# Optimization experiments

Measured on AMD Instinct MI355X. Metric: run time of the kernel, lower is better.

## Reference

```python
import jax, jax.numpy as jnp
import numpy as np

N = 5
C = 256
B, H, W = 8, 64, 64


def setup_inputs() -> dict:
    key = jax.random.key(0)
    ks = jax.random.split(key, 9)
    s = 0.05
    return {
        "inputs": jax.random.normal(ks[0], (B, N, C, H, W), dtype=jnp.float32),
        # grouped 1x1 conv: groups = N-1, each group maps C channels -> 1 channel, no bias
        "wgt_w": jax.random.normal(ks[1], (N - 1, C), dtype=jnp.float32) * s,
        # ConvGRU 1x1 gate convs: in = 2*C (cat of input and hidden), out = C, with bias
        "w_r": jax.random.normal(ks[2], (C, 2 * C), dtype=jnp.float32) * s,
        "b_r": jnp.zeros((C,), dtype=jnp.float32),
        "w_u": jax.random.normal(ks[3], (C, 2 * C), dtype=jnp.float32) * s,
        "b_u": jnp.zeros((C,), dtype=jnp.float32),
        "w_o": jax.random.normal(ks[4], (C, 2 * C), dtype=jnp.float32) * s,
        "b_o": jnp.zeros((C,), dtype=jnp.float32),
        "gamma": jax.random.normal(ks[5], (1,), dtype=jnp.float32) * s,
    }


def _conv1x1(x, Wm, bias):
    # x: [b, cin, h, w]; Wm: [cout, cin]
    return jnp.einsum("bchw,oc->bohw", x, Wm) + bias[None, :, None, None]


def reference(inputs, wgt_w, w_r, b_r, w_u, b_u, w_o, b_o, gamma):
    b, n, c, h, w = inputs.shape

    def gru(x, hprev):
        s = jnp.concatenate([x, hprev], axis=1)  # [b, 2c, h, w]
        u = jax.nn.sigmoid(_conv1x1(s, w_u, b_u))
        r = jax.nn.sigmoid(_conv1x1(s, w_r, b_r))
        o = jnp.tanh(_conv1x1(jnp.concatenate([x, hprev * r], axis=1), w_o, b_o))
        return hprev * (1.0 - u) + o * u

    preds = []
    for i in range(n):
        h_t = inputs[:, i]  # [b, c, h, w]
        idx = [j for j in range(n) if j != i]
        h_n = inputs[:, jnp.array(idx)]  # [b, n-1, c, h, w], neighbor-major channel layout
        diff = h_t[:, None] - h_n  # repeat(h_t, n-1) - cat(neighbors)
        # grouped 1x1 conv (groups = n-1, no bias): per-neighbor channel reduction
        wgt = jnp.einsum("bjchw,jc->bjhw", diff, wgt_w)  # [b, n-1, h, w]
        gate = jax.nn.sigmoid(wgt)
        # torch: wgt.unsqueeze(1).repeat(1, c, 1, 1, 1).view(b, c*(n-1), h, w)
        # -> flat channel index = cc*(n-1) + j  (note: differs from x2's j*c + cc layout)
        gate_full = jnp.broadcast_to(gate[:, None], (b, c, n - 1, h, w)).reshape(
            b, c * (n - 1), h, w
        )
        x2 = h_n.reshape(b, (n - 1) * c, h, w)
        msg = x2 * gate_full
        m_t = msg.reshape(b, n - 1, c, h, w).sum(axis=1)  # sum-aggregate over neighbors
        h_new = gru(m_t, h_t)
        preds.append(h_new * gamma + h_t)
    return jnp.stack(preds, axis=1)  # [b, n, c, h, w]
```

## Files before the change

kernel.cpp:

```cpp
#include <hip/hip_runtime.h>

typedef __attribute__((ext_vector_type(8))) short short8;
typedef __attribute__((ext_vector_type(4))) float f32x4;
typedef __attribute__((ext_vector_type(8))) unsigned short us8;
typedef __attribute__((ext_vector_type(4))) unsigned short us4;
typedef __attribute__((ext_vector_type(2))) unsigned short us2;

__device__ __forceinline__ float sigmoidf_(float x){ return 1.f/(1.f+__expf(-x)); }
__device__ __forceinline__ unsigned short f2bf(float f){
    union{float f; unsigned int u;} x; x.f = f;
    unsigned int r = x.u + 0x7fffu + ((x.u>>16)&1u);
    return (unsigned short)(r>>16);
}
__device__ __forceinline__ float bf2f(unsigned short u){
    union{unsigned int u; float f;} x; x.u = ((unsigned int)u)<<16; return x.f;
}
#define GAS(p) ((const __attribute__((address_space(1))) void*)(uintptr_t)(p))
#define LAS(p) ((__attribute__((address_space(3))) void*)(uintptr_t)(p))

#define SLOT 8388608ull

__global__ __launch_bounds__(256) void k_dots(const float* __restrict__ inp, const float* __restrict__ wgt,
                                              float* __restrict__ D){
    __shared__ float wg[1024];
    for (int s=threadIdx.x; s<1024; s+=256) wg[s] = wgt[s];
    __syncthreads();
    int e = blockIdx.x*256 + threadIdx.x;
    int pl = e & 4095;
    int bn = e >> 12;
    const float* base = inp + (((size_t)bn*256)<<12) + pl;
    float d0=0,d1=0,d2=0,d3=0;
    #pragma unroll 8
    for (int c=0;c<256;c++){
        float v = base[(size_t)c<<12];
        d0 += v*wg[c]; d1 += v*wg[256+c]; d2 += v*wg[512+c]; d3 += v*wg[768+c];
    }
    size_t o = ((size_t)bn*4)<<12;
    D[o+pl]=d0; D[o+4096+pl]=d1; D[o+8192+pl]=d2; D[o+12288+pl]=d3;
}

__global__ __launch_bounds__(256) void k_wp2(const float* __restrict__ w_u, const float* __restrict__ w_r,
                                             const float* __restrict__ w_o,
                                             unsigned short* __restrict__ Wc0, unsigned short* __restrict__ Wc1){
    int bx = blockIdx.x;
    const float *s0, *s1; unsigned short* dst; int OCN, tid;
    if (bx < 256){ tid = bx*256 + threadIdx.x; OCN = 512; s0 = w_u; s1 = w_r; dst = Wc0; }
    else         { tid = (bx-256)*256 + threadIdx.x; OCN = 256; s0 = w_o; s1 = w_o; dst = Wc1; }
    int d = tid*4;
    int kk = d & 63;
    int row = d >> 6;
    int oc = row & (OCN-1);
    int kb = row / OCN;
    int k  = kb*64 + kk;
    const float* src = (oc < 256) ? s0 : s1;
    int ocr = (oc < 256) ? oc : oc-256;
    float4 v = *(const float4*)&src[(size_t)ocr*512 + k];
    us4 pk; pk.x=f2bf(v.x); pk.y=f2bf(v.y); pk.z=f2bf(v.z); pk.w=f2bf(v.w);
    *(us4*)&dst[d] = pk;
}

__global__ __launch_bounds__(256) void k_bxs(const float* __restrict__ inp, const float* __restrict__ D,
                                             unsigned short* __restrict__ Alo, unsigned short* __restrict__ Ahi,
                                             int i0, int cnt){
    __shared__ unsigned short tm[64*34];
    __shared__ unsigned short th[64*34];
    int t  = threadIdx.x;
    int c0 = (blockIdx.x & 3) << 6;
    int pz = blockIdx.x >> 2;
    int p0 = pz << 5;
    int b  = p0 >> 12, pl0 = p0 & 4095;

    f32x4 x[5][2], S4[2];
    #pragma unroll
    for (int q=0;q<2;q++){
        int s = t + q*256;
        int c = s >> 3, pc = (s&7) << 2;
        int cc = c0 + c;
        f32x4 acc = {0.f,0.f,0.f,0.f};
        #pragma unroll
        for (int n=0;n<5;n++){
            x[n][q] = *(const f32x4*)&inp[(((size_t)((b*5+n)*256+cc))<<12) + pl0 + pc];
            acc += x[n][q];
        }
        S4[q] = acc;
    }
    int kb = c0 >> 6;
    #pragma unroll
    for (int i=0;i<5;i++){
        if (i < i0 || i >= i0+cnt) continue;
        #pragma unroll
        for (int q=0;q<2;q++){
            int s = t + q*256;
            int c = s >> 3, pc = (s&7) << 2;
            int j = c & 3;
            int node = (j < i) ? j : (j+1);
            f32x4 dw = *(const f32x4*)&D[(((size_t)((b*5+i)*4+j))<<12) + pl0 + pc];
            f32x4 dn = *(const f32x4*)&D[(((size_t)((b*5+node)*4+j))<<12) + pl0 + pc];
            f32x4 xi = x[i][q];
            f32x4 md = S4[q] - xi;
            int lb = c*34 + pc;
            us2 m0, m1, h0, h1;
            m0.x = f2bf(sigmoidf_(dw.x-dn.x)*md.x); m0.y = f2bf(sigmoidf_(dw.y-dn.y)*md.y);
            m1.x = f2bf(sigmoidf_(dw.z-dn.z)*md.z); m1.y = f2bf(sigmoidf_(dw.w-dn.w)*md.w);
            h0.x = f2bf(xi.x); h0.y = f2bf(xi.y); h1.x = f2bf(xi.z); h1.y = f2bf(xi.w);
            *(us2*)&tm[lb] = m0; *(us2*)&tm[lb+2] = m1;
            *(us2*)&th[lb] = h0; *(us2*)&th[lb+2] = h1;
        }
        __syncthreads();
        {
            int p = t >> 3, cs = (t&7) << 3;
            us8 vm, vh;
            #pragma unroll
            for (int j8=0;j8<8;j8++){ vm[j8] = tm[(cs+j8)*34 + p]; vh[j8] = th[(cs+j8)*34 + p]; }
            size_t dst = (size_t)(i - i0)*SLOT + ((size_t)kb*32768 + p0 + p)*64 + cs;
            *(us8*)&Alo[dst] = vm;
            *(us8*)&Ahi[dst] = vh;
        }
        __syncthreads();
    }
}

template<int EPI>
__global__ __launch_bounds__(256) void k_mm(
        const unsigned short* __restrict__ Alo, const unsigned short* __restrict__ Ahi,
        const unsigned short* __restrict__ Wb,
        const float* __restrict__ inp, const float* __restrict__ b0, const float* __restrict__ b1,
        unsigned short* __restrict__ U, unsigned short* __restrict__ A1hi, float* __restrict__ outp,
        const float* __restrict__ gamma_p, int i0)
{
    constexpr int OCN = EPI ? 256 : 512;
    __shared__ unsigned short As[128*64];
    __shared__ unsigned short Bs[128*64];
    int t  = threadIdx.x, wv = t>>6, ln = t&63;
    int p0 = blockIdx.x*128, oc0 = blockIdx.y*128;
    int z  = blockIdx.z, i = i0 + z;
    size_t zo = (size_t)z*SLOT;
    int wm = (wv>>1)*64, wn = (wv&1)*64;
    int row = ln & 15, quad = ln >> 4, kq = quad*8;

    f32x4 acc[4][4];
    f32x4 zr = {0.f,0.f,0.f,0.f};
    #pragma unroll
    for (int a=0;a<4;a++){
        #pragma unroll
        for (int o=0;o<4;o++) acc[a][o]=zr;
    }

    for (int kb=0; kb<8; ++kb){
        const unsigned short* gA = (kb<4) ? (Alo + zo + ((size_t)kb*32768 + p0)*64)
                                          : (Ahi + zo + ((size_t)(kb-4)*32768 + p0)*64);
        const unsigned short* gW = Wb + ((size_t)kb*OCN + oc0)*64;
        #pragma unroll
        for (int q=0;q<4;q++){
            int off = (wv*4+q)*512;
            __builtin_amdgcn_global_load_lds(GAS(gA + off + ln*8), LAS(Bs + off + ln*8), 16, 0, 0);
            __builtin_amdgcn_global_load_lds(GAS(gW + off + ln*8), LAS(As + off + ln*8), 16, 0, 0);
        }
        __syncthreads();
        #pragma unroll
        for (int ks=0; ks<2; ks++){
            short8 a[4], b[4];
            #pragma unroll
            for (int f=0; f<4; f++){
                a[f] = *(const short8*)&As[(wm+f*16+row)*64 + ks*32 + kq];
                b[f] = *(const short8*)&Bs[(wn+f*16+row)*64 + ks*32 + kq];
            }
            #pragma unroll
            for (int fm=0; fm<4; fm++){
                #pragma unroll
                for (int fn=0; fn<4; fn++)
                    acc[fm][fn] = __builtin_amdgcn_mfma_f32_16x16x32_bf16(a[fm], b[fn], acc[fm][fn], 0,0,0);
            }
        }
        __syncthreads();
    }

    float gm = EPI ? gamma_p[0] : 0.f;
    #pragma unroll
    for (int fn=0; fn<4; fn++){
        int p  = p0 + wn + fn*16 + row;
        int b  = p >> 12, pl = p & 4095;
        size_t hb = (((size_t)((b*5+i)*256))<<12) + pl;
        #pragma unroll
        for (int fm=0; fm<4; fm++){
            int ocb = oc0 + wm + fm*16 + quad*4;
            if (EPI==0){
                if (oc0 < 256){
                    #pragma unroll
                    for (int r=0;r<4;r++){
                        int oc = ocb + r;
                        U[zo + (size_t)oc*32768 + p] = f2bf(sigmoidf_(acc[fm][fn][r] + b0[oc]));
                    }
                } else {
                    int kb2 = ocb - 256;
                    size_t aidx = zo + ((size_t)(kb2>>6)*32768 + p)*64 + (kb2&63);
                    us4 vh = *(const us4*)&Ahi[aidx];
                    us4 pk;
                    #pragma unroll
                    for (int r=0;r<4;r++){
                        float rg = sigmoidf_(acc[fm][fn][r] + b1[kb2+r]);
                        pk[r] = f2bf(rg * bf2f(vh[r]));
                    }
                    *(us4*)&A1hi[aidx] = pk;
                }
            } else {
                #pragma unroll
                for (int r=0;r<4;r++){
                    int oc = ocb + r;
                    float v  = acc[fm][fn][r] + b0[oc];
                    float e2 = __expf(2.f*v);
                    float thv = 1.f - 2.f/(e2+1.f);
                    float u  = bf2f(U[zo + (size_t)oc*32768 + p]);
                    float h  = inp[hb + ((size_t)oc<<12)];
                    float hn = h*(1.f-u) + thv*u;
                    outp[hb + ((size_t)oc<<12)] = hn*gm + h;
                }
            }
        }
    }
}

extern "C" void kernel_launch(void* const* d_in, const int* in_sizes, int n_in,
                              void* d_out, int out_size, void* d_ws, size_t ws_size,
                              hipStream_t stream) {
    const float* inputs = (const float*)d_in[0];
    const float* wgt_w  = (const float*)d_in[1];
    const float* w_r    = (const float*)d_in[2];
    const float* b_r    = (const float*)d_in[3];
    const float* w_u    = (const float*)d_in[4];
    const float* b_u    = (const float*)d_in[5];
    const float* w_o    = (const float*)d_in[6];
    const float* b_o    = (const float*)d_in[7];
    const float* gamma  = (const float*)d_in[8];
    float* out = (float*)d_out;

    float* D = (float*)d_ws;
    unsigned short* Wc0 = (unsigned short*)(D + 655360);
    unsigned short* Wc1 = Wc0 + 262144;
    unsigned short* U   = Wc1 + 131072;

    size_t fixedB = 655360ull*4 + (262144ull + 131072ull)*2;
    size_t slotB  = 4ull*SLOT*2;
    int nb = 1;
    for (int k2=5;k2>=1;k2--){ if (fixedB + (size_t)k2*slotB <= ws_size){ nb = k2; break; } }

    unsigned short* Alo  = U   + (size_t)nb*SLOT;
    unsigned short* Ahi  = Alo + (size_t)nb*SLOT;
    unsigned short* A1hi = Ahi + (size_t)nb*SLOT;

    k_dots<<<640, 256, 0, stream>>>(inputs, wgt_w, D);
    k_wp2 <<<384, 256, 0, stream>>>(w_u, w_r, w_o, Wc0, Wc1);
    for (int i0=0; i0<5; i0+=nb){
        int cnt = (5-i0 < nb) ? (5-i0) : nb;
        k_bxs<<<4096, 256, 0, stream>>>(inputs, D, Alo, Ahi, i0, cnt);
        k_mm<0><<<dim3(256,4,cnt), 256, 0, stream>>>(Alo, Ahi, Wc0, inputs, b_u, b_r,
                                                     U, A1hi, nullptr, gamma, i0);
        k_mm<1><<<dim3(256,2,cnt), 256, 0, stream>>>(Alo, A1hi, Wc1, inputs, b_o, nullptr,
                                                     U, nullptr, out, gamma, i0);
    }
}
```

Before: 872.9 us.

## Double-buffer GEMM LDS tiles, XOR-swizzle layouts, remap blocks across XCDs, vectorize U

The GEMM kernel now double-buffers its LDS tiles so the next K-block loads while MFMAs run, and raises wave priority around the MFMA bursts. The weight and activation panels are XOR-swizzled when written, with matching swizzled LDS reads, to cut bank conflicts. A 1D grid is remapped so consecutive work tiles land on the same XCD, for better L2 sharing of operands. The U gate buffer is transposed to pixel-major so it can be stored and loaded as packed 4-wide vectors. Together these double LDS use and add index arithmetic, and any mismatch between writer and reader swizzles would produce wrong results.

```diff
diff --git a/kernel.cpp b/kernel.cpp
--- a/kernel.cpp
+++ b/kernel.cpp
@@ -56,7 +56,8 @@
     int ocr = (oc < 256) ? oc : oc-256;
     float4 v = *(const float4*)&src[(size_t)ocr*512 + k];
     us4 pk; pk.x=f2bf(v.x); pk.y=f2bf(v.y); pk.z=f2bf(v.z); pk.w=f2bf(v.w);
-    *(us4*)&dst[d] = pk;
+    int kk_sw = kk ^ ((oc&7)<<3);
+    *(us4*)&dst[(size_t)row*64 + kk_sw] = pk;
 }
 
 __global__ __launch_bounds__(256) void k_bxs(const float* __restrict__ inp, const float* __restrict__ D,
@@ -112,7 +113,8 @@
             us8 vm, vh;
             #pragma unroll
             for (int j8=0;j8<8;j8++){ vm[j8] = tm[(cs+j8)*34 + p]; vh[j8] = th[(cs+j8)*34 + p]; }
-            size_t dst = (size_t)(i - i0)*SLOT + ((size_t)kb*32768 + p0 + p)*64 + cs;
+            int cs_sw = cs ^ ((p&7)<<3);
+            size_t dst = (size_t)(i - i0)*SLOT + ((size_t)kb*32768 + p0 + p)*64 + cs_sw;
             *(us8*)&Alo[dst] = vm;
             *(us8*)&Ahi[dst] = vh;
         }
@@ -129,10 +131,17 @@
         const float* __restrict__ gamma_p, int i0)
 {
     constexpr int OCN = EPI ? 256 : 512;
-    __shared__ unsigned short As[128*64];
-    __shared__ unsigned short Bs[128*64];
+    constexpr int NY  = EPI ? 2   : 4;
+    constexpr int NWG = 256*NY;
+    __shared__ unsigned short As[2][128*64];
+    __shared__ unsigned short Bs[2][128*64];
     int t  = threadIdx.x, wv = t>>6, ln = t&63;
-    int p0 = blockIdx.x*128, oc0 = blockIdx.y*128;
+
+    int bid = blockIdx.x;
+    int wg  = (bid&7)*(NWG>>3) + (bid>>3);
+    int oc0 = (wg & (NY-1)) * 128;
+    int p0  = (wg / NY) * 128;
+
     int z  = blockIdx.z, i = i0 + z;
     size_t zo = (size_t)z*SLOT;
     int wm = (wv>>1)*64, wn = (wv&1)*64;
@@ -146,31 +155,42 @@
         for (int o=0;o<4;o++) acc[a][o]=zr;
     }
 
-    for (int kb=0; kb<8; ++kb){
+    auto stage = [&](int kb, int buf){
         const unsigned short* gA = (kb<4) ? (Alo + zo + ((size_t)kb*32768 + p0)*64)
                                           : (Ahi + zo + ((size_t)(kb-4)*32768 + p0)*64);
         const unsigned short* gW = Wb + ((size_t)kb*OCN + oc0)*64;
         #pragma unroll
         for (int q=0;q<4;q++){
             int off = (wv*4+q)*512;
-            __builtin_amdgcn_global_load_lds(GAS(gA + off + ln*8), LAS(Bs + off + ln*8), 16, 0, 0);
-            __builtin_amdgcn_global_load_lds(GAS(gW + off + ln*8), LAS(As + off + ln*8), 16, 0, 0);
-        }
-        __syncthreads();
+            __builtin_amdgcn_global_load_lds(GAS(gA + off + ln*8), LAS(&Bs[buf][off + ln*8]), 16, 0, 0);
+            __builtin_amdgcn_global_load_lds(GAS(gW + off + ln*8), LAS(&As[buf][off + ln*8]), 16, 0, 0);
+        }
+    };
+
+    stage(0, 0);
+    __syncthreads();
+
+    int rsw = (row&7)<<3;
+    for (int kb=0; kb<8; ++kb){
+        int cur = kb & 1;
+        if (kb < 7) stage(kb+1, cur^1);
         #pragma unroll
         for (int ks=0; ks<2; ks++){
             short8 a[4], b[4];
+            int col = (ks*32 + kq) ^ rsw;
             #pragma unroll
             for (int f=0; f<4; f++){
-                a[f] = *(const short8*)&As[(wm+f*16+row)*64 + ks*32 + kq];
-                b[f] = *(const short8*)&Bs[(wn+f*16+row)*64 + ks*32 + kq];
+                a[f] = *(const short8*)&As[cur][(wm+f*16+row)*64 + col];
+                b[f] = *(const short8*)&Bs[cur][(wn+f*16+row)*64 + col];
             }
+            __builtin_amdgcn_s_setprio(1);
             #pragma unroll
             for (int fm=0; fm<4; fm++){
                 #pragma unroll
                 for (int fn=0; fn<4; fn++)
                     acc[fm][fn] = __builtin_amdgcn_mfma_f32_16x16x32_bf16(a[fm], b[fn], acc[fm][fn], 0,0,0);
             }
+            __builtin_amdgcn_s_setprio(0);
         }
         __syncthreads();
     }
@@ -186,14 +206,15 @@
             int ocb = oc0 + wm + fm*16 + quad*4;
             if (EPI==0){
                 if (oc0 < 256){
+                    us4 pk;
                     #pragma unroll
-                    for (int r=0;r<4;r++){
-                        int oc = ocb + r;
-                        U[zo + (size_t)oc*32768 + p] = f2bf(sigmoidf_(acc[fm][fn][r] + b0[oc]));
-                    }
+                    for (int r=0;r<4;r++)
+                        pk[r] = f2bf(sigmoidf_(acc[fm][fn][r] + b0[ocb+r]));
+                    *(us4*)&U[zo + (size_t)p*256 + ocb] = pk;
                 } else {
                     int kb2 = ocb - 256;
-                    size_t aidx = zo + ((size_t)(kb2>>6)*32768 + p)*64 + (kb2&63);
+                    int kc  = (kb2&63) ^ ((p&7)<<3);
+                    size_t aidx = zo + ((size_t)(kb2>>6)*32768 + p)*64 + kc;
                     us4 vh = *(const us4*)&Ahi[aidx];
                     us4 pk;
                     #pragma unroll
@@ -204,13 +225,14 @@
                     *(us4*)&A1hi[aidx] = pk;
                 }
             } else {
+                us4 vu = *(const us4*)&U[zo + (size_t)p*256 + ocb];
                 #pragma unroll
                 for (int r=0;r<4;r++){
                     int oc = ocb + r;
                     float v  = acc[fm][fn][r] + b0[oc];
                     float e2 = __expf(2.f*v);
                     float thv = 1.f - 2.f/(e2+1.f);
-                    float u  = bf2f(U[zo + (size_t)oc*32768 + p]);
+                    float u  = bf2f(vu[r]);
                     float h  = inp[hb + ((size_t)oc<<12)];
                     float hn = h*(1.f-u) + thv*u;
                     outp[hb + ((size_t)oc<<12)] = hn*gm + h;
@@ -253,9 +275,9 @@
     for (int i0=0; i0<5; i0+=nb){
         int cnt = (5-i0 < nb) ? (5-i0) : nb;
         k_bxs<<<4096, 256, 0, stream>>>(inputs, D, Alo, Ahi, i0, cnt);
-        k_mm<0><<<dim3(256,4,cnt), 256, 0, stream>>>(Alo, Ahi, Wc0, inputs, b_u, b_r,
-                                                     U, A1hi, nullptr, gamma, i0);
-        k_mm<1><<<dim3(256,2,cnt), 256, 0, stream>>>(Alo, A1hi, Wc1, inputs, b_o, nullptr,
+        k_mm<0><<<dim3(1024,1,cnt), 256, 0, stream>>>(Alo, Ahi, Wc0, inputs, b_u, b_r,
+                                                      U, A1hi, nullptr, gamma, i0);
+        k_mm<1><<<dim3(512,1,cnt), 256, 0, stream>>>(Alo, A1hi, Wc1, inputs, b_o, nullptr,
                                                      U, nullptr, out, gamma, i0);
     }
 }
```

New measurement: 707.6 us. 18.9% less time.
